# Optimization experiments

Measured on AMD Instinct MI355X. Metric: run time of the kernel, lower is better.

## Reference

```python
import jax, jax.numpy as jnp
import numpy as np

NEG_SLOPE = 0.2   # RGATConv default negative_slope
BN_EPS = 1e-5     # torch BatchNorm1d default eps


def _build_edges(n0, n1, batch):
    """Replicates generate_edges_union + PyG Batch offsetting. Returns [2, B*E] src/dst and [B*E] edge types."""
    n = n0 + n1
    def perm(k, off):  # itertools.permutations(range(k), 2) as (src, dst) columns
        a = np.repeat(np.arange(k), k); b = np.tile(np.arange(k), k)
        m = a != b
        return np.stack([a[m], b[m]]) + off
    intra = np.concatenate([perm(n0, 0), perm(n1, n0)], axis=1)                 # edge_type 0
    ca = np.repeat(np.arange(n0), n1); cb = np.tile(np.arange(n0, n), n0)
    cross = np.concatenate([np.stack([ca, cb]), np.stack([cb, ca])], axis=1)    # edge_type 1
    edges = np.concatenate([intra, cross], axis=1)
    etype = np.concatenate([np.zeros(intra.shape[1], np.int32), np.ones(cross.shape[1], np.int32)])
    offs = (np.arange(batch) * n)[:, None, None]
    edges_b = (edges[None, :, :] + offs).transpose(1, 0, 2).reshape(2, -1)      # per-graph node offsets
    etype_b = np.tile(etype, batch)
    return jnp.asarray(edges_b, jnp.int32), jnp.asarray(etype_b, jnp.int32)


def _segment_softmax(logits, seg, num_seg):
    m = jax.ops.segment_max(logits, seg, num_segments=num_seg)
    m = jnp.where(jnp.isfinite(m), m, 0.0)
    e = jnp.exp(logits - m[seg])
    s = jax.ops.segment_sum(e, seg, num_segments=num_seg)
    return e / (s[seg] + 1e-16)  # PyG softmax eps


def _rgat_layer(x, src, dst, etype, W, q, k, b, num_nodes):
    # PyG RGATConv: heads=1, dim=1, concat=False, additive-self-attention, across-relation softmax, aggr=add
    H = jnp.einsum('nf,rfe->rne', x, W)            # relation-specific transform: [2, BN, F]
    qs = jnp.einsum('rne,e->rn', H, q)             # q-score per node per relation
    ks = jnp.einsum('rne,e->rn', H, k)
    logit = jax.nn.leaky_relu(qs[etype, dst] + ks[etype, src], NEG_SLOPE)  # [E]
    alpha = _segment_softmax(logit, dst, num_nodes)
    msg = alpha[:, None] * H[etype, src]           # [E, F] per-edge messages
    out = jax.ops.segment_sum(msg, dst, num_segments=num_nodes)
    return out + b                                 # heads=1 -> mean over heads is identity; + bias


def setup_inputs() -> dict:
    key = jax.random.key(0)
    ks = jax.random.split(key, 6)
    B, F, N0, N1, L = 4, 256, 128, 128, 3
    s = 0.05
    return {
        'desc0': jax.random.normal(ks[0], (B, F, N0), jnp.float32),
        'desc1': jax.random.normal(ks[1], (B, F, N1), jnp.float32),
        'conv_w': jax.random.normal(ks[2], (L, 2, F, F), jnp.float32) * s,
        'conv_q': jax.random.normal(ks[3], (L, F), jnp.float32) * s,
        'conv_k': jax.random.normal(ks[4], (L, F), jnp.float32) * s,
        'conv_b': jnp.zeros((L, F), jnp.float32),
        'lin_w': jax.random.normal(ks[5], (L, F, 2 * F), jnp.float32) * s,
        'lin_b': jnp.zeros((L, F), jnp.float32),
        'bn_w': jnp.ones((L, F), jnp.float32),
        'bn_b': jnp.zeros((L, F), jnp.float32),
    }


def reference(desc0, desc1, conv_w, conv_q, conv_k, conv_b, lin_w, lin_b, bn_w, bn_b):
    b, f, n0 = desc0.shape
    n1 = desc1.shape[2]
    n = n0 + n1
    # [B, F, N] -> batched node features [B*N, F]
    x = jnp.concatenate([desc0, desc1], axis=2).transpose(0, 2, 1).reshape(b * n, f)
    edges, etype = _build_edges(n0, n1, b)
    src, dst = edges[0], edges[1]
    num_nodes = b * n
    for i in range(conv_w.shape[0]):
        msg1 = jax.nn.relu(_rgat_layer(x, src, dst, etype, conv_w[i], conv_q[i], conv_k[i], conv_b[i], num_nodes))
        msg2 = jnp.concatenate([x, msg1], axis=1) @ lin_w[i].T + lin_b[i]
        mu = msg2.mean(axis=0)
        var = msg2.var(axis=0)  # biased, as torch BatchNorm uses for normalization (training mode)
        msg3 = bn_w[i] * (msg2 - mu) / jnp.sqrt(var + BN_EPS) + bn_b[i]
        x = x + msg3            # edge_pool[i] == 1 -> no knn_graph rebuild
    x = x.reshape(b, n, f).transpose(0, 2, 1)
    return x[:, :, :n0], x[:, :, n0:]
```

## Files before the change

### kernel.cpp

```cpp
#include <hip/hip_runtime.h>
#include <math.h>


typedef __attribute__((ext_vector_type(8))) short short8;
typedef __attribute__((ext_vector_type(4))) float f32x4;
typedef unsigned short u16;
typedef unsigned int   u32;

__device__ __forceinline__ u16 f2bf(float f) {
    union { float f; u32 u; } v; v.f = f;
    u32 r = v.u + 0x7fffu + ((v.u >> 16) & 1u);
    return (u16)(r >> 16);
}
__device__ __forceinline__ short8 ld8(const u16* p) {
    return __builtin_bit_cast(short8, *(const int4*)p);
}

__global__ __launch_bounds__(256) void k_prep(
    const float* __restrict__ d0, const float* __restrict__ d1,
    const float* __restrict__ conv_w, const float* __restrict__ lin_w,
    float* __restrict__ x, u16* __restrict__ xb,
    u16* __restrict__ Wt, u16* __restrict__ lwb) {
    const int t = threadIdx.x;
    if (blockIdx.x < 256) {
        __shared__ float Ts[32 * 33];
        const int tt = blockIdx.x;
        const int b = tt >> 6, rem = tt & 63, ft = rem >> 3, nt = rem & 7;
        const float* src = (nt < 4) ? d0 : d1;
        const int nloc = (nt & 3) * 32;
        {
            int fr = t >> 3, c4 = t & 7;
            float4 v = *(const float4*)&src[b * 32768 + (ft * 32 + fr) * 128 + nloc + c4 * 4];
            Ts[fr * 33 + c4 * 4 + 0] = v.x;
            Ts[fr * 33 + c4 * 4 + 1] = v.y;
            Ts[fr * 33 + c4 * 4 + 2] = v.z;
            Ts[fr * 33 + c4 * 4 + 3] = v.w;
        }
        __syncthreads();
        {
            int nr = t >> 3, f4 = t & 7;
            float4 v;
            v.x = Ts[(f4 * 4 + 0) * 33 + nr];
            v.y = Ts[(f4 * 4 + 1) * 33 + nr];
            v.z = Ts[(f4 * 4 + 2) * 33 + nr];
            v.w = Ts[(f4 * 4 + 3) * 33 + nr];
            int node = b * 256 + nt * 32 + nr;
            int idx = node * 256 + ft * 32 + f4 * 4;
            *(float4*)&x[idx] = v;
            ushort4 hb = {f2bf(v.x), f2bf(v.y), f2bf(v.z), f2bf(v.w)};
            *(ushort4*)&xb[idx] = hb;
        }
    } else if (blockIdx.x < 640) {
        __shared__ float Ts[32 * 33];
        const int tt = blockIdx.x - 256;
        const int mat = tt >> 6, rem = tt & 63, et = rem >> 3, ft = rem & 7;
        {
            int fr = t >> 3, c4 = t & 7;
            float4 v = *(const float4*)&conv_w[mat * 65536 + (ft * 32 + fr) * 256 + et * 32 + c4 * 4];
            Ts[fr * 33 + c4 * 4 + 0] = v.x;
            Ts[fr * 33 + c4 * 4 + 1] = v.y;
            Ts[fr * 33 + c4 * 4 + 2] = v.z;
            Ts[fr * 33 + c4 * 4 + 3] = v.w;
        }
        __syncthreads();
        {
            int er = t >> 3, f4 = t & 7;
            ushort4 hb;
            hb.x = f2bf(Ts[(f4 * 4 + 0) * 33 + er]);
            hb.y = f2bf(Ts[(f4 * 4 + 1) * 33 + er]);
            hb.z = f2bf(Ts[(f4 * 4 + 2) * 33 + er]);
            hb.w = f2bf(Ts[(f4 * 4 + 3) * 33 + er]);
            *(ushort4*)&Wt[mat * 65536 + (et * 32 + er) * 256 + ft * 32 + f4 * 4] = hb;
        }
    } else {
        int o4 = (blockIdx.x - 640) * 256 + t;
        float4 v = *(const float4*)&lin_w[o4 * 4];
        ushort4 hb = {f2bf(v.x), f2bf(v.y), f2bf(v.z), f2bf(v.w)};
        *(ushort4*)&lwb[o4 * 4] = hb;
    }
}

__global__ __launch_bounds__(256, 1) void k_hqk(
    const float* __restrict__ xprev, const float* __restrict__ msg2,
    const float* __restrict__ gsum, const float* __restrict__ gsumsq,
    const float* __restrict__ bw, const float* __restrict__ bb,
    const u16* __restrict__ cwt,
    const float* __restrict__ cq, const float* __restrict__ ck,
    float* __restrict__ xcur, u16* __restrict__ xb, u16* __restrict__ Ht,
    float* __restrict__ qpart, float* __restrict__ kpart, int do_bn) {
    __shared__ __align__(16) u16 Asub[16 * 264];
    __shared__ __align__(16) float sc[256];
    __shared__ __align__(16) float sh[256];
    const int tid = threadIdx.x;
    const int mt = blockIdx.x >> 3, sg = blockIdx.x & 7;
    const int rel = sg >> 2, eg = sg & 3;
    const int m0 = mt * 16;
    const int lane = tid & 63, widx = tid >> 6;
    const int row = lane & 15, kg = lane >> 4;

    if (do_bn) {
        float s1 = gsum[tid], s2 = gsumsq[tid];
        float mu  = s1 * (1.f / 1024.f);
        float var = s2 * (1.f / 1024.f) - mu * mu;
        float scale = bw[tid] * rsqrtf(var + 1e-5f);
        sc[tid] = scale;
        sh[tid] = bb[tid] - mu * scale;
    }
    __syncthreads();
    #pragma unroll
    for (int p = 0; p < 4; ++p) {
        const int r = p * 4 + (tid >> 6);
        const int c0 = (tid & 63) * 4;
        const int idx = (m0 + r) * 256 + c0;
        float4 v = *(const float4*)&xprev[idx];
        if (do_bn) {
            float4 m = *(const float4*)&msg2[idx];
            float4 s4 = *(const float4*)&sc[c0];
            float4 h4 = *(const float4*)&sh[c0];
            v.x += m.x * s4.x + h4.x;
            v.y += m.y * s4.y + h4.y;
            v.z += m.z * s4.z + h4.z;
            v.w += m.w * s4.w + h4.w;
        }
        ushort4 hb = {f2bf(v.x), f2bf(v.y), f2bf(v.z), f2bf(v.w)};
        *(ushort4*)&Asub[r * 264 + c0] = hb;
        if (do_bn && sg == 0) {
            *(float4*)&xcur[idx] = v;
            *(ushort4*)&xb[idx] = hb;
        }
    }
    __syncthreads();

    const int et = eg * 4 + widx, e0 = et * 16;
    const u16* B = cwt + rel * 65536 + (e0 + row) * 256 + kg * 8;
    const u16* Ap = &Asub[row * 264 + kg * 8];
    f32x4 acc = {0.f,0.f,0.f,0.f};
    #pragma unroll
    for (int k0 = 0; k0 < 256; k0 += 32)
        acc = __builtin_amdgcn_mfma_f32_16x16x32_bf16(ld8(Ap + k0), ld8(B + k0), acc, 0, 0, 0);
    ushort4 o0;
    o0.x = f2bf(acc[0]); o0.y = f2bf(acc[1]); o0.z = f2bf(acc[2]); o0.w = f2bf(acc[3]);
    *(ushort4*)(Ht + rel * 262144 + (e0 + row) * 1024 + m0 + kg * 4) = o0;
    float qe = cq[e0 + row], ke = ck[e0 + row];
    float pq[4], pk[4];
    #pragma unroll
    for (int c = 0; c < 4; ++c) { pq[c] = acc[c] * qe; pk[c] = acc[c] * ke; }
    #pragma unroll
    for (int off = 1; off < 16; off <<= 1) {
        #pragma unroll
        for (int c = 0; c < 4; ++c) {
            pq[c] += __shfl_xor(pq[c], off);
            pk[c] += __shfl_xor(pk[c], off);
        }
    }
    if (row == 0) {
        float4 a4 = {pq[0], pq[1], pq[2], pq[3]};
        float4 b4 = {pk[0], pk[1], pk[2], pk[3]};
        *(float4*)&qpart[(rel * 16 + et) * 1024 + m0 + kg * 4] = a4;
        *(float4*)&kpart[(rel * 16 + et) * 1024 + m0 + kg * 4] = b4;
    }
}

__global__ __launch_bounds__(256, 1) void k_attn(
    const float* __restrict__ qpart, const float* __restrict__ kpart,
    const u16* __restrict__ Ht, const float* __restrict__ cb,
    u16* __restrict__ msg1b, float* __restrict__ gsum, float* __restrict__ gsumsq) {
    __shared__ __align__(16) u16 Atile[16 * 264];
    __shared__ float ksl[2][256];
    __shared__ float qsl[2][16];
    __shared__ __align__(16) float T[4][16 * 20];
    const int tid = threadIdx.x;
    const int mt = blockIdx.x >> 2, eg = blockIdx.x & 3;
    const int m0 = mt * 16;
    const int g = mt >> 4, a = (mt >> 3) & 1;
    if (blockIdx.x == 0) { gsum[tid] = 0.f; gsumsq[tid] = 0.f; }
    {
        float k0s = 0.f, k1s = 0.f;
        #pragma unroll
        for (int c = 0; c < 16; ++c) {
            k0s += kpart[c * 1024 + g * 256 + tid];
            k1s += kpart[(16 + c) * 1024 + g * 256 + tid];
        }
        ksl[0][tid] = k0s; ksl[1][tid] = k1s;
    }
    if (tid < 32) {
        int rel = tid >> 4, r = tid & 15;
        float q = 0.f;
        #pragma unroll
        for (int c = 0; c < 16; ++c) q += qpart[(rel * 16 + c) * 1024 + m0 + r];
        qsl[rel][r] = q;
    }
    __syncthreads();
    {
        const int r = tid >> 4, j = tid & 15;
        const int dl = (m0 + r) & 255;
        const int s0 = j * 16;
        const int rel = ((s0 >> 7) == a) ? 0 : 1;
        float qv = qsl[rel][r];
        float l[16], mx = -1e30f;
        #pragma unroll
        for (int i2 = 0; i2 < 16; ++i2) {
            float v = qv + ksl[rel][s0 + i2];
            v = (v >= 0.f) ? v : 0.2f * v;
            if (s0 + i2 == dl) v = -1e30f;
            l[i2] = v; mx = fmaxf(mx, v);
        }
        #pragma unroll
        for (int off = 1; off < 16; off <<= 1) mx = fmaxf(mx, __shfl_xor(mx, off));
        float s = 0.f;
        #pragma unroll
        for (int i2 = 0; i2 < 16; ++i2) { l[i2] = __expf(l[i2] - mx); s += l[i2]; }
        #pragma unroll
        for (int off = 1; off < 16; off <<= 1) s += __shfl_xor(s, off);
        float inv = 1.f / (s + 1e-16f);
        #pragma unroll
        for (int i2 = 0; i2 < 16; i2 += 2) {
            u32 p = (u32)f2bf(l[i2] * inv) | ((u32)f2bf(l[i2 + 1] * inv) << 16);
            *(u32*)&Atile[r * 264 + s0 + i2] = p;
        }
    }
    __syncthreads();
    const int lane = tid & 63, widx = tid >> 6;
    const int row = lane & 15, kg = lane >> 4;
    const int et = eg * 4 + widx, e0 = et * 16;
    const u16* Ap = &Atile[row * 264 + kg * 8];
    f32x4 acc = {0.f,0.f,0.f,0.f};
    #pragma unroll
    for (int k0 = 0; k0 < 256; k0 += 32) {
        const int rel = (((k0 >> 7) & 1) == a) ? 0 : 1;
        const u16* B = Ht + rel * 262144 + (e0 + row) * 1024 + g * 256 + k0 + kg * 8;
        acc = __builtin_amdgcn_mfma_f32_16x16x32_bf16(ld8(Ap + k0), ld8(B), acc, 0, 0, 0);
    }
    float bias = cb[e0 + row];
    float* Tw = &T[widx][0];
    #pragma unroll
    for (int c = 0; c < 4; ++c)
        Tw[(kg * 4 + c) * 20 + row] = fmaxf(acc[c] + bias, 0.f);
    __syncthreads();
    float4 v = *(float4*)&Tw[row * 20 + kg * 4];
    u32 lo = (u32)f2bf(v.x) | ((u32)f2bf(v.y) << 16);
    u32 hi = (u32)f2bf(v.z) | ((u32)f2bf(v.w) << 16);
    uint2 ov = {lo, hi};
    *(uint2*)(msg1b + (m0 + row) * 256 + e0 + kg * 4) = ov;
}

__global__ __launch_bounds__(128, 1) void k_lin(
    const u16* __restrict__ xb, const u16* __restrict__ msg1b,
    const u16* __restrict__ lwp, const float* __restrict__ lb,
    float* __restrict__ msg2, float* __restrict__ gsum, float* __restrict__ gsumsq) {
    __shared__ __align__(16) float T[2][16 * 20];
    const int tid = threadIdx.x, lane = tid & 63, widx = tid >> 6;
    const int row = lane & 15, kg = lane >> 4;
    const int mt = blockIdx.x >> 3, ng = blockIdx.x & 7;
    const int m0 = mt * 16;
    const int n0 = (ng * 2 + widx) * 16;
    const u16* A0 = xb    + (m0 + row) * 256 + kg * 8;
    const u16* A1 = msg1b + (m0 + row) * 256 + kg * 8;
    const u16* B  = lwp + (n0 + row) * 512 + kg * 8;
    f32x4 acc = {0.f,0.f,0.f,0.f};
    #pragma unroll
    for (int k0 = 0; k0 < 512; k0 += 32) {
        short8 av = (k0 < 256) ? ld8(A0 + k0) : ld8(A1 + (k0 - 256));
        acc = __builtin_amdgcn_mfma_f32_16x16x32_bf16(av, ld8(B + k0), acc, 0, 0, 0);
    }
    float bias = lb[n0 + row];
    float v0 = acc[0] + bias, v1 = acc[1] + bias, v2 = acc[2] + bias, v3 = acc[3] + bias;
    float s1 = v0 + v1 + v2 + v3;
    float s2 = v0 * v0 + v1 * v1 + v2 * v2 + v3 * v3;
    s1 += __shfl_xor(s1, 16); s1 += __shfl_xor(s1, 32);
    s2 += __shfl_xor(s2, 16); s2 += __shfl_xor(s2, 32);
    if (lane < 16) {
        atomicAdd(&gsum[n0 + lane], s1);
        atomicAdd(&gsumsq[n0 + lane], s2);
    }
    float* Tw = &T[widx][0];
    Tw[(kg * 4 + 0) * 20 + row] = v0;
    Tw[(kg * 4 + 1) * 20 + row] = v1;
    Tw[(kg * 4 + 2) * 20 + row] = v2;
    Tw[(kg * 4 + 3) * 20 + row] = v3;
    float4 vv = *(float4*)&Tw[row * 20 + kg * 4];
    *(float4*)&msg2[(m0 + row) * 256 + n0 + kg * 4] = vv;
}

__global__ __launch_bounds__(256) void k_fin(
    const float* __restrict__ x2, const float* __restrict__ msg2,
    const float* __restrict__ gsum, const float* __restrict__ gsumsq,
    const float* __restrict__ bw, const float* __restrict__ bb,
    float* __restrict__ out) {
    __shared__ float Tt[32 * 33];
    __shared__ float scf[32];
    __shared__ float shf[32];
    const int t = threadIdx.x;
    const int nt2 = blockIdx.x >> 3, ft = blockIdx.x & 7;
    const int n0 = nt2 * 32, f0 = ft * 32;
    if (t < 32) {
        float s1 = gsum[f0 + t], s2 = gsumsq[f0 + t];
        float mu  = s1 * (1.f / 1024.f);
        float var = s2 * (1.f / 1024.f) - mu * mu;
        float scale = bw[f0 + t] * rsqrtf(var + 1e-5f);
        scf[t] = scale;
        shf[t] = bb[f0 + t] - mu * scale;
    }
    __syncthreads();
    {
        const int nr = t >> 3, f4 = t & 7;
        const int idx = (n0 + nr) * 256 + f0 + f4 * 4;
        float4 v = *(const float4*)&x2[idx];
        float4 m = *(const float4*)&msg2[idx];
        v.x += m.x * scf[f4 * 4 + 0] + shf[f4 * 4 + 0];
        v.y += m.y * scf[f4 * 4 + 1] + shf[f4 * 4 + 1];
        v.z += m.z * scf[f4 * 4 + 2] + shf[f4 * 4 + 2];
        v.w += m.w * scf[f4 * 4 + 3] + shf[f4 * 4 + 3];
        Tt[(f4 * 4 + 0) * 33 + nr] = v.x;
        Tt[(f4 * 4 + 1) * 33 + nr] = v.y;
        Tt[(f4 * 4 + 2) * 33 + nr] = v.z;
        Tt[(f4 * 4 + 3) * 33 + nr] = v.w;
    }
    __syncthreads();
    {
        const int fr = t >> 3, n4 = t & 7;
        const int b = n0 >> 8, half = (n0 >> 7) & 1, nloc = n0 & 127;
        float4 v;
        v.x = Tt[fr * 33 + n4 * 4 + 0];
        v.y = Tt[fr * 33 + n4 * 4 + 1];
        v.z = Tt[fr * 33 + n4 * 4 + 2];
        v.w = Tt[fr * 33 + n4 * 4 + 3];
        *(float4*)&out[half * 131072 + b * 32768 + (f0 + fr) * 128 + nloc + n4 * 4] = v;
    }
}

extern "C" void kernel_launch(void* const* d_in, const int* in_sizes, int n_in,
                              void* d_out, int out_size, void* d_ws, size_t ws_size,
                              hipStream_t stream) {
    const float* desc0  = (const float*)d_in[0];
    const float* desc1  = (const float*)d_in[1];
    const float* conv_w = (const float*)d_in[2];
    const float* conv_q = (const float*)d_in[3];
    const float* conv_k = (const float*)d_in[4];
    const float* conv_b = (const float*)d_in[5];
    const float* lin_w  = (const float*)d_in[6];
    const float* lin_b  = (const float*)d_in[7];
    const float* bn_w   = (const float*)d_in[8];
    const float* bn_b   = (const float*)d_in[9];
    float* out = (float*)d_out;

    char* p = (char*)d_ws;
    float* x0     = (float*)p; p += 1048576;
    float* x1     = (float*)p; p += 1048576;
    u16*   xb     = (u16*)p;   p += 524288;
    u16*   Wt     = (u16*)p;   p += 786432;
    u16*   lwb    = (u16*)p;   p += 786432;
    u16*   Ht     = (u16*)p;   p += 1048576;
    float* qpart  = (float*)p; p += 131072;
    float* kpart  = (float*)p; p += 131072;
    u16*   msg1b  = (u16*)p;   p += 524288;
    float* msg2   = (float*)p; p += 1048576;
    float* gsum   = (float*)p; p += 1024;
    float* gsumsq = (float*)p; p += 1024;

    k_prep<<<1024, 256, 0, stream>>>(desc0, desc1, conv_w, lin_w, x0, xb, Wt, lwb);

    float* xs[4] = {x0, x0, x1, x0};
    for (int i = 0; i < 3; ++i) {
        const u16*   cwt = Wt + i * 131072;
        const u16*   lwp = lwb + i * 131072;
        const float* cq = conv_q + i * 256;
        const float* ck = conv_k + i * 256;
        const float* cb = conv_b + i * 256;
        const float* lb = lin_b + i * 256;
        const float* bwp = bn_w + (i ? (i - 1) * 256 : 0);
        const float* bbp = bn_b + (i ? (i - 1) * 256 : 0);

        k_hqk<<<512, 256, 0, stream>>>(xs[i], msg2, gsum, gsumsq, bwp, bbp,
                                       cwt, cq, ck, xs[i + 1], xb, Ht,
                                       qpart, kpart, i > 0 ? 1 : 0);
        k_attn<<<256, 256, 0, stream>>>(qpart, kpart, Ht, cb, msg1b, gsum, gsumsq);
        k_lin<<<512, 128, 0, stream>>>(xb, msg1b, lwp, lb, msg2, gsum, gsumsq);
    }

    k_fin<<<256, 256, 0, stream>>>(xs[3], msg2, gsum, gsumsq,
                                   bn_w + 512, bn_b + 512, out);
}
```

Measured before the change: 138.4 us.

## Fuse attention aggregation and linear layer into one kernel per layer

Result: slower. 156.0 us (+12.7%).

```diff
diff --git a/kernel.cpp b/kernel.cpp
--- a/kernel.cpp
+++ b/kernel.cpp
@@ -20,7 +20,7 @@
     const float* __restrict__ d0, const float* __restrict__ d1,
     const float* __restrict__ conv_w, const float* __restrict__ lin_w,
     float* __restrict__ x, u16* __restrict__ xb,
-    u16* __restrict__ Wt, u16* __restrict__ lwb) {
+    u16* __restrict__ Wt, u16* __restrict__ lwb, float* __restrict__ gz) {
     const int t = threadIdx.x;
     if (blockIdx.x < 256) {
         __shared__ float Ts[32 * 33];
@@ -77,6 +77,10 @@
         float4 v = *(const float4*)&lin_w[o4 * 4];
         ushort4 hb = {f2bf(v.x), f2bf(v.y), f2bf(v.z), f2bf(v.w)};
         *(ushort4*)&lwb[o4 * 4] = hb;
+        if (blockIdx.x == 640) {
+            #pragma unroll
+            for (int j = 0; j < 6; ++j) gz[j * 256 + t] = 0.f;
+        }
     }
 }
 
@@ -161,19 +165,21 @@
     }
 }
 
-__global__ __launch_bounds__(256, 1) void k_attn(
+__global__ __launch_bounds__(256, 1) void k_attn_lin(
     const float* __restrict__ qpart, const float* __restrict__ kpart,
     const u16* __restrict__ Ht, const float* __restrict__ cb,
-    u16* __restrict__ msg1b, float* __restrict__ gsum, float* __restrict__ gsumsq) {
+    const u16* __restrict__ xb, const u16* __restrict__ lwp,
+    const float* __restrict__ lb,
+    float* __restrict__ msg2, float* __restrict__ gsum, float* __restrict__ gsumsq) {
     __shared__ __align__(16) u16 Atile[16 * 264];
+    __shared__ __align__(16) u16 M1[16 * 264];
     __shared__ float ksl[2][256];
     __shared__ float qsl[2][16];
     __shared__ __align__(16) float T[4][16 * 20];
     const int tid = threadIdx.x;
-    const int mt = blockIdx.x >> 2, eg = blockIdx.x & 3;
+    const int mt = blockIdx.x >> 2, nq = blockIdx.x & 3;
     const int m0 = mt * 16;
     const int g = mt >> 4, a = (mt >> 3) & 1;
-    if (blockIdx.x == 0) { gsum[tid] = 0.f; gsumsq[tid] = 0.f; }
     {
         float k0s = 0.f, k1s = 0.f;
         #pragma unroll
@@ -222,46 +228,38 @@
     __syncthreads();
     const int lane = tid & 63, widx = tid >> 6;
     const int row = lane & 15, kg = lane >> 4;
-    const int et = eg * 4 + widx, e0 = et * 16;
     const u16* Ap = &Atile[row * 264 + kg * 8];
-    f32x4 acc = {0.f,0.f,0.f,0.f};
-    #pragma unroll
-    for (int k0 = 0; k0 < 256; k0 += 32) {
-        const int rel = (((k0 >> 7) & 1) == a) ? 0 : 1;
-        const u16* B = Ht + rel * 262144 + (e0 + row) * 1024 + g * 256 + k0 + kg * 8;
-        acc = __builtin_amdgcn_mfma_f32_16x16x32_bf16(ld8(Ap + k0), ld8(B), acc, 0, 0, 0);
-    }
-    float bias = cb[e0 + row];
     float* Tw = &T[widx][0];
     #pragma unroll
-    for (int c = 0; c < 4; ++c)
-        Tw[(kg * 4 + c) * 20 + row] = fmaxf(acc[c] + bias, 0.f);
-    __syncthreads();
-    float4 v = *(float4*)&Tw[row * 20 + kg * 4];
-    u32 lo = (u32)f2bf(v.x) | ((u32)f2bf(v.y) << 16);
-    u32 hi = (u32)f2bf(v.z) | ((u32)f2bf(v.w) << 16);
-    uint2 ov = {lo, hi};
-    *(uint2*)(msg1b + (m0 + row) * 256 + e0 + kg * 4) = ov;
-}
-
-__global__ __launch_bounds__(128, 1) void k_lin(
-    const u16* __restrict__ xb, const u16* __restrict__ msg1b,
-    const u16* __restrict__ lwp, const float* __restrict__ lb,
-    float* __restrict__ msg2, float* __restrict__ gsum, float* __restrict__ gsumsq) {
-    __shared__ __align__(16) float T[2][16 * 20];
-    const int tid = threadIdx.x, lane = tid & 63, widx = tid >> 6;
-    const int row = lane & 15, kg = lane >> 4;
-    const int mt = blockIdx.x >> 3, ng = blockIdx.x & 7;
-    const int m0 = mt * 16;
-    const int n0 = (ng * 2 + widx) * 16;
-    const u16* A0 = xb    + (m0 + row) * 256 + kg * 8;
-    const u16* A1 = msg1b + (m0 + row) * 256 + kg * 8;
-    const u16* B  = lwp + (n0 + row) * 512 + kg * 8;
+    for (int c4 = 0; c4 < 4; ++c4) {
+        const int e0 = (widx * 4 + c4) * 16;
+        f32x4 acc = {0.f,0.f,0.f,0.f};
+        #pragma unroll
+        for (int k0 = 0; k0 < 256; k0 += 32) {
+            const int rel = (((k0 >> 7) & 1) == a) ? 0 : 1;
+            const u16* B = Ht + rel * 262144 + (e0 + row) * 1024 + g * 256 + k0 + kg * 8;
+            acc = __builtin_amdgcn_mfma_f32_16x16x32_bf16(ld8(Ap + k0), ld8(B), acc, 0, 0, 0);
+        }
+        float bias = cb[e0 + row];
+        #pragma unroll
+        for (int c = 0; c < 4; ++c)
+            Tw[(kg * 4 + c) * 20 + row] = fmaxf(acc[c] + bias, 0.f);
+        float4 v = *(float4*)&Tw[row * 20 + kg * 4];
+        u32 lo = (u32)f2bf(v.x) | ((u32)f2bf(v.y) << 16);
+        u32 hi = (u32)f2bf(v.z) | ((u32)f2bf(v.w) << 16);
+        uint2 ov = {lo, hi};
+        *(uint2*)&M1[row * 264 + e0 + kg * 4] = ov;
+    }
+    __syncthreads();
+    const int n0 = (nq * 4 + widx) * 16;
+    const u16* A0 = xb + (m0 + row) * 256 + kg * 8;
+    const u16* A1 = &M1[row * 264 + kg * 8];
+    const u16* Bl = lwp + (n0 + row) * 512 + kg * 8;
     f32x4 acc = {0.f,0.f,0.f,0.f};
     #pragma unroll
     for (int k0 = 0; k0 < 512; k0 += 32) {
         short8 av = (k0 < 256) ? ld8(A0 + k0) : ld8(A1 + (k0 - 256));
-        acc = __builtin_amdgcn_mfma_f32_16x16x32_bf16(av, ld8(B + k0), acc, 0, 0, 0);
+        acc = __builtin_amdgcn_mfma_f32_16x16x32_bf16(av, ld8(Bl + k0), acc, 0, 0, 0);
     }
     float bias = lb[n0 + row];
     float v0 = acc[0] + bias, v1 = acc[1] + bias, v2 = acc[2] + bias, v3 = acc[3] + bias;
@@ -273,7 +271,6 @@
         atomicAdd(&gsum[n0 + lane], s1);
         atomicAdd(&gsumsq[n0 + lane], s2);
     }
-    float* Tw = &T[widx][0];
     Tw[(kg * 4 + 0) * 20 + row] = v0;
     Tw[(kg * 4 + 1) * 20 + row] = v1;
     Tw[(kg * 4 + 2) * 20 + row] = v2;
@@ -353,12 +350,11 @@
     u16*   Ht     = (u16*)p;   p += 1048576;
     float* qpart  = (float*)p; p += 131072;
     float* kpart  = (float*)p; p += 131072;
-    u16*   msg1b  = (u16*)p;   p += 524288;
     float* msg2   = (float*)p; p += 1048576;
-    float* gsum   = (float*)p; p += 1024;
-    float* gsumsq = (float*)p; p += 1024;
-
-    k_prep<<<1024, 256, 0, stream>>>(desc0, desc1, conv_w, lin_w, x0, xb, Wt, lwb);
+    float* gsA    = (float*)p; p += 3072;
+    float* gqA    = (float*)p; p += 3072;
+
+    k_prep<<<1024, 256, 0, stream>>>(desc0, desc1, conv_w, lin_w, x0, xb, Wt, lwb, gsA);
 
     float* xs[4] = {x0, x0, x1, x0};
     for (int i = 0; i < 3; ++i) {
@@ -370,14 +366,16 @@
         const float* lb = lin_b + i * 256;
         const float* bwp = bn_w + (i ? (i - 1) * 256 : 0);
         const float* bbp = bn_b + (i ? (i - 1) * 256 : 0);
-
-        k_hqk<<<512, 256, 0, stream>>>(xs[i], msg2, gsum, gsumsq, bwp, bbp,
+        const float* gsp = gsA + (i ? (i - 1) * 256 : 0);
+        const float* gqp = gqA + (i ? (i - 1) * 256 : 0);
+
+        k_hqk<<<512, 256, 0, stream>>>(xs[i], msg2, gsp, gqp, bwp, bbp,
                                        cwt, cq, ck, xs[i + 1], xb, Ht,
                                        qpart, kpart, i > 0 ? 1 : 0);
-        k_attn<<<256, 256, 0, stream>>>(qpart, kpart, Ht, cb, msg1b, gsum, gsumsq);
-        k_lin<<<512, 128, 0, stream>>>(xb, msg1b, lwp, lb, msg2, gsum, gsumsq);
-    }
-
-    k_fin<<<256, 256, 0, stream>>>(xs[3], msg2, gsum, gsumsq,
+        k_attn_lin<<<256, 256, 0, stream>>>(qpart, kpart, Ht, cb, xb, lwp, lb,
+                                            msg2, gsA + i * 256, gqA + i * 256);
+    }
+
+    k_fin<<<256, 256, 0, stream>>>(xs[3], msg2, gsA + 512, gqA + 512,
                                    bn_w + 512, bn_b + 512, out);
 }
```

## Fuse per-layer kernels into one cooperative persistent kernel with grid syncs

Applied to the files above, without the earlier changes.

New measurement: 417.3 us. 201% more time.

```diff
diff --git a/kernel.cpp b/kernel.cpp
--- a/kernel.cpp
+++ b/kernel.cpp
@@ -1,6 +1,9 @@
 #include <hip/hip_runtime.h>
+#include <hip/hip_cooperative_groups.h>
 #include <math.h>
 
+
+namespace cg = cooperative_groups;
 
 typedef __attribute__((ext_vector_type(8))) short short8;
 typedef __attribute__((ext_vector_type(4))) float f32x4;
@@ -16,11 +19,17 @@
     return __builtin_bit_cast(short8, *(const int4*)p);
 }
 
+struct SmemHqk  { u16 Asub[16 * 264]; float sc[256]; float sh[256]; };
+struct SmemAttn { u16 Atile[16 * 264]; float ksl[2][256]; float qsl[2][16]; float T[4][16 * 20]; };
+struct SmemLin  { float T[4][16 * 20]; };
+struct SmemFin  { float Tt[32 * 33]; float scf[32]; float shf[32]; };
+union  SmemU { SmemHqk h; SmemAttn a; SmemLin l; SmemFin f; };
+
 __global__ __launch_bounds__(256) void k_prep(
     const float* __restrict__ d0, const float* __restrict__ d1,
     const float* __restrict__ conv_w, const float* __restrict__ lin_w,
     float* __restrict__ x, u16* __restrict__ xb,
-    u16* __restrict__ Wt, u16* __restrict__ lwb) {
+    u16* __restrict__ Wt, u16* __restrict__ lwb, float* __restrict__ gz) {
     const int t = threadIdx.x;
     if (blockIdx.x < 256) {
         __shared__ float Ts[32 * 33];
@@ -77,23 +86,25 @@
         float4 v = *(const float4*)&lin_w[o4 * 4];
         ushort4 hb = {f2bf(v.x), f2bf(v.y), f2bf(v.z), f2bf(v.w)};
         *(ushort4*)&lwb[o4 * 4] = hb;
-    }
-}
-
-__global__ __launch_bounds__(256, 1) void k_hqk(
+        if (blockIdx.x == 640) {
+            #pragma unroll
+            for (int j = 0; j < 6; ++j) gz[j * 256 + t] = 0.f;
+        }
+    }
+}
+
+__device__ __forceinline__ void stage_hqk(
+    SmemHqk& s, int b,
     const float* __restrict__ xprev, const float* __restrict__ msg2,
     const float* __restrict__ gsum, const float* __restrict__ gsumsq,
     const float* __restrict__ bw, const float* __restrict__ bb,
-    const u16* __restrict__ cwt,
-    const float* __restrict__ cq, const float* __restrict__ ck,
+    const u16* __restrict__ cwt, const float* __restrict__ cq,
+    const float* __restrict__ ck,
     float* __restrict__ xcur, u16* __restrict__ xb, u16* __restrict__ Ht,
     float* __restrict__ qpart, float* __restrict__ kpart, int do_bn) {
-    __shared__ __align__(16) u16 Asub[16 * 264];
-    __shared__ __align__(16) float sc[256];
-    __shared__ __align__(16) float sh[256];
     const int tid = threadIdx.x;
-    const int mt = blockIdx.x >> 3, sg = blockIdx.x & 7;
-    const int rel = sg >> 2, eg = sg & 3;
+    const int mt = b >> 2, pr = b & 3;
+    const int rel = pr >> 1;
     const int m0 = mt * 16;
     const int lane = tid & 63, widx = tid >> 6;
     const int row = lane & 15, kg = lane >> 4;
@@ -103,8 +114,8 @@
         float mu  = s1 * (1.f / 1024.f);
         float var = s2 * (1.f / 1024.f) - mu * mu;
         float scale = bw[tid] * rsqrtf(var + 1e-5f);
-        sc[tid] = scale;
-        sh[tid] = bb[tid] - mu * scale;
+        s.sc[tid] = scale;
+        s.sh[tid] = bb[tid] - mu * scale;
     }
     __syncthreads();
     #pragma unroll
@@ -115,65 +126,65 @@
         float4 v = *(const float4*)&xprev[idx];
         if (do_bn) {
             float4 m = *(const float4*)&msg2[idx];
-            float4 s4 = *(const float4*)&sc[c0];
-            float4 h4 = *(const float4*)&sh[c0];
+            float4 s4 = *(const float4*)&s.sc[c0];
+            float4 h4 = *(const float4*)&s.sh[c0];
             v.x += m.x * s4.x + h4.x;
             v.y += m.y * s4.y + h4.y;
             v.z += m.z * s4.z + h4.z;
             v.w += m.w * s4.w + h4.w;
         }
         ushort4 hb = {f2bf(v.x), f2bf(v.y), f2bf(v.z), f2bf(v.w)};
-        *(ushort4*)&Asub[r * 264 + c0] = hb;
-        if (do_bn && sg == 0) {
+        *(ushort4*)&s.Asub[r * 264 + c0] = hb;
+        if (do_bn && pr == 0) {
             *(float4*)&xcur[idx] = v;
             *(ushort4*)&xb[idx] = hb;
         }
     }
     __syncthreads();
 
-    const int et = eg * 4 + widx, e0 = et * 16;
-    const u16* B = cwt + rel * 65536 + (e0 + row) * 256 + kg * 8;
-    const u16* Ap = &Asub[row * 264 + kg * 8];
-    f32x4 acc = {0.f,0.f,0.f,0.f};
+    const u16* Ap = &s.Asub[row * 264 + kg * 8];
     #pragma unroll
-    for (int k0 = 0; k0 < 256; k0 += 32)
-        acc = __builtin_amdgcn_mfma_f32_16x16x32_bf16(ld8(Ap + k0), ld8(B + k0), acc, 0, 0, 0);
-    ushort4 o0;
-    o0.x = f2bf(acc[0]); o0.y = f2bf(acc[1]); o0.z = f2bf(acc[2]); o0.w = f2bf(acc[3]);
-    *(ushort4*)(Ht + rel * 262144 + (e0 + row) * 1024 + m0 + kg * 4) = o0;
-    float qe = cq[e0 + row], ke = ck[e0 + row];
-    float pq[4], pk[4];
-    #pragma unroll
-    for (int c = 0; c < 4; ++c) { pq[c] = acc[c] * qe; pk[c] = acc[c] * ke; }
-    #pragma unroll
-    for (int off = 1; off < 16; off <<= 1) {
-        #pragma unroll
-        for (int c = 0; c < 4; ++c) {
-            pq[c] += __shfl_xor(pq[c], off);
-            pk[c] += __shfl_xor(pk[c], off);
-        }
-    }
-    if (row == 0) {
-        float4 a4 = {pq[0], pq[1], pq[2], pq[3]};
-        float4 b4 = {pk[0], pk[1], pk[2], pk[3]};
-        *(float4*)&qpart[(rel * 16 + et) * 1024 + m0 + kg * 4] = a4;
-        *(float4*)&kpart[(rel * 16 + et) * 1024 + m0 + kg * 4] = b4;
-    }
-}
-
-__global__ __launch_bounds__(256, 1) void k_attn(
+    for (int egi = 0; egi < 2; ++egi) {
+        const int eg = (pr & 1) * 2 + egi;
+        const int et = eg * 4 + widx, e0 = et * 16;
+        const u16* B = cwt + rel * 65536 + (e0 + row) * 256 + kg * 8;
+        f32x4 acc = {0.f,0.f,0.f,0.f};
+        #pragma unroll
+        for (int k0 = 0; k0 < 256; k0 += 32)
+            acc = __builtin_amdgcn_mfma_f32_16x16x32_bf16(ld8(Ap + k0), ld8(B + k0), acc, 0, 0, 0);
+        ushort4 o0;
+        o0.x = f2bf(acc[0]); o0.y = f2bf(acc[1]); o0.z = f2bf(acc[2]); o0.w = f2bf(acc[3]);
+        *(ushort4*)(Ht + rel * 262144 + (e0 + row) * 1024 + m0 + kg * 4) = o0;
+        float qe = cq[e0 + row], ke = ck[e0 + row];
+        float pq[4], pk[4];
+        #pragma unroll
+        for (int c = 0; c < 4; ++c) { pq[c] = acc[c] * qe; pk[c] = acc[c] * ke; }
+        #pragma unroll
+        for (int off = 1; off < 16; off <<= 1) {
+            #pragma unroll
+            for (int c = 0; c < 4; ++c) {
+                pq[c] += __shfl_xor(pq[c], off);
+                pk[c] += __shfl_xor(pk[c], off);
+            }
+        }
+        if (row == 0) {
+            float4 a4 = {pq[0], pq[1], pq[2], pq[3]};
+            float4 b4 = {pk[0], pk[1], pk[2], pk[3]};
+            *(float4*)&qpart[(rel * 16 + et) * 1024 + m0 + kg * 4] = a4;
+            *(float4*)&kpart[(rel * 16 + et) * 1024 + m0 + kg * 4] = b4;
+        }
+    }
+}
+
+__device__ __forceinline__ void stage_attn(
+    SmemAttn& s, int vb,
     const float* __restrict__ qpart, const float* __restrict__ kpart,
     const u16* __restrict__ Ht, const float* __restrict__ cb,
-    u16* __restrict__ msg1b, float* __restrict__ gsum, float* __restrict__ gsumsq) {
-    __shared__ __align__(16) u16 Atile[16 * 264];
-    __shared__ float ksl[2][256];
-    __shared__ float qsl[2][16];
-    __shared__ __align__(16) float T[4][16 * 20];
+    u16* __restrict__ msg1b) {
     const int tid = threadIdx.x;
-    const int mt = blockIdx.x >> 2, eg = blockIdx.x & 3;
+    const int mt = vb >> 2, eg = vb & 3;
     const int m0 = mt * 16;
     const int g = mt >> 4, a = (mt >> 3) & 1;
-    if (blockIdx.x == 0) { gsum[tid] = 0.f; gsumsq[tid] = 0.f; }
     {
         float k0s = 0.f, k1s = 0.f;
         #pragma unroll
@@ -181,14 +192,14 @@
             k0s += kpart[c * 1024 + g * 256 + tid];
             k1s += kpart[(16 + c) * 1024 + g * 256 + tid];
         }
-        ksl[0][tid] = k0s; ksl[1][tid] = k1s;
+        s.ksl[0][tid] = k0s; s.ksl[1][tid] = k1s;
     }
     if (tid < 32) {
         int rel = tid >> 4, r = tid & 15;
         float q = 0.f;
         #pragma unroll
         for (int c = 0; c < 16; ++c) q += qpart[(rel * 16 + c) * 1024 + m0 + r];
-        qsl[rel][r] = q;
+        s.qsl[rel][r] = q;
     }
     __syncthreads();
     {
@@ -196,34 +207,34 @@
         const int dl = (m0 + r) & 255;
         const int s0 = j * 16;
         const int rel = ((s0 >> 7) == a) ? 0 : 1;
-        float qv = qsl[rel][r];
+        float qv = s.qsl[rel][r];
         float l[16], mx = -1e30f;
         #pragma unroll
         for (int i2 = 0; i2 < 16; ++i2) {
-            float v = qv + ksl[rel][s0 + i2];
+            float v = qv + s.ksl[rel][s0 + i2];
             v = (v >= 0.f) ? v : 0.2f * v;
             if (s0 + i2 == dl) v = -1e30f;
             l[i2] = v; mx = fmaxf(mx, v);
         }
         #pragma unroll
         for (int off = 1; off < 16; off <<= 1) mx = fmaxf(mx, __shfl_xor(mx, off));
-        float s = 0.f;
-        #pragma unroll
-        for (int i2 = 0; i2 < 16; ++i2) { l[i2] = __expf(l[i2] - mx); s += l[i2]; }
-        #pragma unroll
-        for (int off = 1; off < 16; off <<= 1) s += __shfl_xor(s, off);
-        float inv = 1.f / (s + 1e-16f);
+        float sum = 0.f;
+        #pragma unroll
+        for (int i2 = 0; i2 < 16; ++i2) { l[i2] = __expf(l[i2] - mx); sum += l[i2]; }
+        #pragma unroll
+        for (int off = 1; off < 16; off <<= 1) sum += __shfl_xor(sum, off);
+        float inv = 1.f / (sum + 1e-16f);
         #pragma unroll
         for (int i2 = 0; i2 < 16; i2 += 2) {
-            u32 p = (u32)f2bf(l[i2] * inv) | ((u32)f2bf(l[i2 + 1] * inv) << 16);
-            *(u32*)&Atile[r * 264 + s0 + i2] = p;
+            u32 pk2 = (u32)f2bf(l[i2] * inv) | ((u32)f2bf(l[i2 + 1] * inv) << 16);
+            *(u32*)&s.Atile[r * 264 + s0 + i2] = pk2;
         }
     }
     __syncthreads();
     const int lane = tid & 63, widx = tid >> 6;
     const int row = lane & 15, kg = lane >> 4;
     const int et = eg * 4 + widx, e0 = et * 16;
-    const u16* Ap = &Atile[row * 264 + kg * 8];
+    const u16* Ap = &s.Atile[row * 264 + kg * 8];
     f32x4 acc = {0.f,0.f,0.f,0.f};
     #pragma unroll
     for (int k0 = 0; k0 < 256; k0 += 32) {
@@ -232,11 +243,10 @@
         acc = __builtin_amdgcn_mfma_f32_16x16x32_bf16(ld8(Ap + k0), ld8(B), acc, 0, 0, 0);
     }
     float bias = cb[e0 + row];
-    float* Tw = &T[widx][0];
+    float* Tw = &s.T[widx][0];
     #pragma unroll
     for (int c = 0; c < 4; ++c)
         Tw[(kg * 4 + c) * 20 + row] = fmaxf(acc[c] + bias, 0.f);
-    __syncthreads();
     float4 v = *(float4*)&Tw[row * 20 + kg * 4];
     u32 lo = (u32)f2bf(v.x) | ((u32)f2bf(v.y) << 16);
     u32 hi = (u32)f2bf(v.z) | ((u32)f2bf(v.w) << 16);
@@ -244,16 +254,17 @@
     *(uint2*)(msg1b + (m0 + row) * 256 + e0 + kg * 4) = ov;
 }
 
-__global__ __launch_bounds__(128, 1) void k_lin(
+__device__ __forceinline__ void stage_lin(
+    SmemLin& s, int b,
     const u16* __restrict__ xb, const u16* __restrict__ msg1b,
     const u16* __restrict__ lwp, const float* __restrict__ lb,
     float* __restrict__ msg2, float* __restrict__ gsum, float* __restrict__ gsumsq) {
-    __shared__ __align__(16) float T[2][16 * 20];
-    const int tid = threadIdx.x, lane = tid & 63, widx = tid >> 6;
+    const int tid = threadIdx.x;
+    const int lane = tid & 63, w = tid >> 6;
     const int row = lane & 15, kg = lane >> 4;
-    const int mt = blockIdx.x >> 3, ng = blockIdx.x & 7;
+    const int mt = b >> 2, q = b & 3;
     const int m0 = mt * 16;
-    const int n0 = (ng * 2 + widx) * 16;
+    const int n0 = (q * 4 + w) * 16;
     const u16* A0 = xb    + (m0 + row) * 256 + kg * 8;
     const u16* A1 = msg1b + (m0 + row) * 256 + kg * 8;
     const u16* B  = lwp + (n0 + row) * 512 + kg * 8;
@@ -273,7 +284,7 @@
         atomicAdd(&gsum[n0 + lane], s1);
         atomicAdd(&gsumsq[n0 + lane], s2);
     }
-    float* Tw = &T[widx][0];
+    float* Tw = &s.T[w][0];
     Tw[(kg * 4 + 0) * 20 + row] = v0;
     Tw[(kg * 4 + 1) * 20 + row] = v1;
     Tw[(kg * 4 + 2) * 20 + row] = v2;
@@ -282,24 +293,22 @@
     *(float4*)&msg2[(m0 + row) * 256 + n0 + kg * 4] = vv;
 }
 
-__global__ __launch_bounds__(256) void k_fin(
+__device__ __forceinline__ void stage_fin(
+    SmemFin& s, int vb,
     const float* __restrict__ x2, const float* __restrict__ msg2,
     const float* __restrict__ gsum, const float* __restrict__ gsumsq,
     const float* __restrict__ bw, const float* __restrict__ bb,
     float* __restrict__ out) {
-    __shared__ float Tt[32 * 33];
-    __shared__ float scf[32];
-    __shared__ float shf[32];
     const int t = threadIdx.x;
-    const int nt2 = blockIdx.x >> 3, ft = blockIdx.x & 7;
+    const int nt2 = vb >> 3, ft = vb & 7;
     const int n0 = nt2 * 32, f0 = ft * 32;
     if (t < 32) {
         float s1 = gsum[f0 + t], s2 = gsumsq[f0 + t];
         float mu  = s1 * (1.f / 1024.f);
         float var = s2 * (1.f / 1024.f) - mu * mu;
         float scale = bw[f0 + t] * rsqrtf(var + 1e-5f);
-        scf[t] = scale;
-        shf[t] = bb[f0 + t] - mu * scale;
+        s.scf[t] = scale;
+        s.shf[t] = bb[f0 + t] - mu * scale;
     }
     __syncthreads();
     {
@@ -307,26 +316,59 @@
         const int idx = (n0 + nr) * 256 + f0 + f4 * 4;
         float4 v = *(const float4*)&x2[idx];
         float4 m = *(const float4*)&msg2[idx];
-        v.x += m.x * scf[f4 * 4 + 0] + shf[f4 * 4 + 0];
-        v.y += m.y * scf[f4 * 4 + 1] + shf[f4 * 4 + 1];
-        v.z += m.z * scf[f4 * 4 + 2] + shf[f4 * 4 + 2];
-        v.w += m.w * scf[f4 * 4 + 3] + shf[f4 * 4 + 3];
-        Tt[(f4 * 4 + 0) * 33 + nr] = v.x;
-        Tt[(f4 * 4 + 1) * 33 + nr] = v.y;
-        Tt[(f4 * 4 + 2) * 33 + nr] = v.z;
-        Tt[(f4 * 4 + 3) * 33 + nr] = v.w;
+        v.x += m.x * s.scf[f4 * 4 + 0] + s.shf[f4 * 4 + 0];
+        v.y += m.y * s.scf[f4 * 4 + 1] + s.shf[f4 * 4 + 1];
+        v.z += m.z * s.scf[f4 * 4 + 2] + s.shf[f4 * 4 + 2];
+        v.w += m.w * s.scf[f4 * 4 + 3] + s.shf[f4 * 4 + 3];
+        s.Tt[(f4 * 4 + 0) * 33 + nr] = v.x;
+        s.Tt[(f4 * 4 + 1) * 33 + nr] = v.y;
+        s.Tt[(f4 * 4 + 2) * 33 + nr] = v.z;
+        s.Tt[(f4 * 4 + 3) * 33 + nr] = v.w;
     }
     __syncthreads();
     {
         const int fr = t >> 3, n4 = t & 7;
         const int b = n0 >> 8, half = (n0 >> 7) & 1, nloc = n0 & 127;
         float4 v;
-        v.x = Tt[fr * 33 + n4 * 4 + 0];
-        v.y = Tt[fr * 33 + n4 * 4 + 1];
-        v.z = Tt[fr * 33 + n4 * 4 + 2];
-        v.w = Tt[fr * 33 + n4 * 4 + 3];
+        v.x = s.Tt[fr * 33 + n4 * 4 + 0];
+        v.y = s.Tt[fr * 33 + n4 * 4 + 1];
+        v.z = s.Tt[fr * 33 + n4 * 4 + 2];
+        v.w = s.Tt[fr * 33 + n4 * 4 + 3];
         *(float4*)&out[half * 131072 + b * 32768 + (f0 + fr) * 128 + nloc + n4 * 4] = v;
     }
+}
+
+__global__ __launch_bounds__(256) void k_mega(
+    const float* __restrict__ conv_q, const float* __restrict__ conv_k,
+    const float* __restrict__ conv_b, const float* __restrict__ lin_b,
+    const float* __restrict__ bn_w, const float* __restrict__ bn_b,
+    float* __restrict__ x0, float* __restrict__ x1,
+    u16* __restrict__ xb, const u16* __restrict__ Wt, const u16* __restrict__ lwb,
+    u16* __restrict__ Ht, float* __restrict__ qpart, float* __restrict__ kpart,
+    u16* __restrict__ msg1b, float* __restrict__ msg2,
+    float* __restrict__ gsA, float* __restrict__ gqA,
+    float* __restrict__ out) {
+    __shared__ __align__(16) SmemU sm;
+    cg::grid_group grid = cg::this_grid();
+    const int b = blockIdx.x;
+    const float* xs_r[3] = {x0, x0, x1};
+    float*       xs_w[3] = {x0, x1, x0};
+    #pragma unroll 1
+    for (int i = 0; i < 3; ++i) {
+        const int po = i ? (i - 1) * 256 : 0;
+        stage_hqk(sm.h, b, xs_r[i], msg2, gsA + po, gqA + po,
+                  bn_w + po, bn_b + po,
+                  Wt + i * 131072, conv_q + i * 256, conv_k + i * 256,
+                  xs_w[i], xb, Ht, qpart, kpart, i > 0 ? 1 : 0);
+        grid.sync();
+        stage_attn(sm.a, b, qpart, kpart, Ht, conv_b + i * 256, msg1b);
+        grid.sync();
+        stage_lin(sm.l, b, xb, msg1b, lwb + i * 131072, lin_b + i * 256,
+                  msg2, gsA + i * 256, gqA + i * 256);
+        grid.sync();
+    }
+    stage_fin(sm.f, b, xs_w[2], msg2, gsA + 512, gqA + 512,
+              bn_w + 512, bn_b + 512, out);
 }
 
 extern "C" void kernel_launch(void* const* d_in, const int* in_sizes, int n_in,
@@ -355,29 +397,19 @@
     float* kpart  = (float*)p; p += 131072;
     u16*   msg1b  = (u16*)p;   p += 524288;
     float* msg2   = (float*)p; p += 1048576;
-    float* gsum   = (float*)p; p += 1024;
-    float* gsumsq = (float*)p; p += 1024;
-
-    k_prep<<<1024, 256, 0, stream>>>(desc0, desc1, conv_w, lin_w, x0, xb, Wt, lwb);
-
-    float* xs[4] = {x0, x0, x1, x0};
-    for (int i = 0; i < 3; ++i) {
-        const u16*   cwt = Wt + i * 131072;
-        const u16*   lwp = lwb + i * 131072;
-        const float* cq = conv_q + i * 256;
-        const float* ck = conv_k + i * 256;
-        const float* cb = conv_b + i * 256;
-        const float* lb = lin_b + i * 256;
-        const float* bwp = bn_w + (i ? (i - 1) * 256 : 0);
-        const float* bbp = bn_b + (i ? (i - 1) * 256 : 0);
-
-        k_hqk<<<512, 256, 0, stream>>>(xs[i], msg2, gsum, gsumsq, bwp, bbp,
-                                       cwt, cq, ck, xs[i + 1], xb, Ht,
-                                       qpart, kpart, i > 0 ? 1 : 0);
-        k_attn<<<256, 256, 0, stream>>>(qpart, kpart, Ht, cb, msg1b, gsum, gsumsq);
-        k_lin<<<512, 128, 0, stream>>>(xb, msg1b, lwp, lb, msg2, gsum, gsumsq);
-    }
-
-    k_fin<<<256, 256, 0, stream>>>(xs[3], msg2, gsum, gsumsq,
-                                   bn_w + 512, bn_b + 512, out);
-}
+    float* gsA    = (float*)p; p += 3072;
+    float* gqA    = (float*)p; p += 3072;
+
+    k_prep<<<1024, 256, 0, stream>>>(desc0, desc1, conv_w, lin_w, x0, xb, Wt, lwb,
+                                     gsA);
+
+    void* kargs[] = {
+        (void*)&conv_q, (void*)&conv_k, (void*)&conv_b, (void*)&lin_b,
+        (void*)&bn_w,   (void*)&bn_b,
+        (void*)&x0,     (void*)&x1,     (void*)&xb,     (void*)&Wt,
+        (void*)&lwb,    (void*)&Ht,     (void*)&qpart,  (void*)&kpart,
+        (void*)&msg1b,  (void*)&msg2,   (void*)&gsA,    (void*)&gqA,
+        (void*)&out,
+    };
+    hipLaunchCooperativeKernel(k_mega, dim3(256), dim3(256), kargs, 0, stream);
+}
```
